# Kernel tuning notes

Hardware: AMD Instinct MI355X
Metric: run time of the kernel (lower is better)

## Reference

```python
import jax, jax.numpy as jnp
import numpy as np

NUM_EXPERTS = 8


def setup_inputs() -> dict:
    key = jax.random.key(0)
    k1, k2, k3, k4, k5 = jax.random.split(key, 5)
    T, D, DFF, E, K = 2048, 2048, 1024, NUM_EXPERTS, 2
    hidden_states = jax.random.normal(k1, (T, D), dtype=jnp.float32)
    w1 = jax.random.normal(k2, (E, 2 * DFF, D), dtype=jnp.float32) * 0.02
    w2 = jax.random.normal(k3, (E, D, DFF), dtype=jnp.float32) * 0.02
    topk_weights = jax.random.uniform(k4, (T, K), dtype=jnp.float32)
    topk_weights = topk_weights / jnp.sum(topk_weights, axis=-1, keepdims=True)
    topk_ids = jax.random.randint(k5, (T, K), 0, E, dtype=jnp.int32)
    return {"hidden_states": hidden_states, "w1": w1, "w2": w2,
            "topk_weights": topk_weights, "topk_ids": topk_ids}


def _expert_fn(x, w1_e, w2_e):
    # x: [T, D], w1_e: [2*DFF, D], w2_e: [D, DFF]
    gu = x @ w1_e.T                      # [T, 2*DFF]
    dff = w2_e.shape[1]
    gate, up = gu[:, :dff], gu[:, dff:]
    h = jax.nn.silu(gate) * up           # SiLU-and-mul activation
    return h @ w2_e.T                    # [T, D]


def reference(hidden_states, w1, w2, topk_weights, topk_ids):
    T = hidden_states.shape[0]
    E = w1.shape[0]
    # route[t, e] = sum_k topk_weights[t,k] * (topk_ids[t,k] == e)
    route = jnp.zeros((T, E), dtype=hidden_states.dtype)
    route = route.at[jnp.arange(T)[:, None], topk_ids].add(topk_weights)
    # per-expert dense GEMMs (E is small and fixed), then weighted combine
    outs = jax.vmap(lambda w1_e, w2_e: _expert_fn(hidden_states, w1_e, w2_e))(w1, w2)  # [E, T, D]
    return jnp.einsum('te,etd->td', route, outs)
```

## Files before the change

kernel.cpp:

```cpp
#include <hip/hip_runtime.h>
#include <hip/hip_bf16.h>
#include <stdint.h>

typedef __attribute__((ext_vector_type(4))) float f32x4;
typedef __attribute__((ext_vector_type(8))) short bf16x8;
typedef unsigned short u16;

#define T_TOK   2048
#define D_DIM   2048
#define DFF_DIM 1024
#define NEXP    8
#define TOPK    2
#define NROWS   (T_TOK * TOPK)
#define BM      128
#define BK      64
#define MAX_MB  40
#define GRID_G  (16 * MAX_MB)
#define CVT2_BLKS 256

#define XB_OFF    65536
#define XB_BYTES  ((size_t)T_TOK * D_DIM * 2)
#define H_OFF     (XB_OFF + XB_BYTES)
#define H_BYTES   ((size_t)NROWS * DFF_DIM * 2)
#define W1B_OFF   (H_OFF + H_BYTES)
#define W1B_BYTES ((size_t)NEXP * 2 * DFF_DIM * D_DIM * 2)
#define W2B_OFF   (W1B_OFF + W1B_BYTES)
#define W2B_BYTES ((size_t)NEXP * D_DIM * DFF_DIM * 2)
#define WS_NEED   (W2B_OFF + W2B_BYTES)

#define W1_T   ((size_t)NEXP * 2 * DFF_DIM * D_DIM / 8)
#define W2_T   ((size_t)NEXP * D_DIM * DFF_DIM / 8)
#define X_T    ((size_t)T_TOK * D_DIM / 8)
#define PREP_CHUNKS_A (W1_T + X_T)
#define PREP_BLKS 2048

#define PIN() asm volatile("" ::: "memory")
#define BAR_LGKM()                                                        \
    asm volatile("s_waitcnt lgkmcnt(0)" ::: "memory");                    \
    __builtin_amdgcn_s_barrier()

__device__ __forceinline__ u16 f2bf(float f) {
    __hip_bfloat16 h = __float2bfloat16(f);
    return *reinterpret_cast<u16*>(&h);
}

__device__ __forceinline__ void cvt8(const float* src, u16* dst) {
    f32x4 a = *(const f32x4*)src;
    f32x4 b = *(const f32x4*)(src + 4);
    bf16x8 v;
#pragma unroll
    for (int j = 0; j < 4; ++j) { v[j] = (short)f2bf(a[j]); v[j + 4] = (short)f2bf(b[j]); }
    *(bf16x8*)dst = v;
}

__device__ __forceinline__ void cvt8_nt(const float* src, u16* dst) {
    f32x4 a = __builtin_nontemporal_load((const f32x4*)src);
    f32x4 b = __builtin_nontemporal_load(((const f32x4*)src) + 1);
    bf16x8 v;
#pragma unroll
    for (int j = 0; j < 4; ++j) { v[j] = (short)f2bf(a[j]); v[j + 4] = (short)f2bf(b[j]); }
    *(bf16x8*)dst = v;
}

__device__ __forceinline__ void gll16(const u16* gsrc, const u16* lds) {
    __builtin_amdgcn_global_load_lds(
        (const __attribute__((address_space(1))) uint32_t*)gsrc,
        (__attribute__((address_space(3))) uint32_t*)lds, 16, 0, 0);
}

__device__ __forceinline__ bf16x8 lds_read8_swz(const u16* base, int row, int inner) {
    int off = row * 128 + (inner ^ ((row & 7) << 4));
    return *(const bf16x8*)((const char*)base + off);
}

__device__ __forceinline__ void route_body(const int* topk_ids, const float* topk_w,
                                           int* sched, int* row_token, float* row_w,
                                           int* cnt, int* off, int* cur) {
    const int tid = threadIdx.x;
    if (tid < NEXP) cnt[tid] = 0;
    __syncthreads();
    for (int p = tid; p < NROWS; p += blockDim.x)
        atomicAdd(&cnt[topk_ids[p]], 1);
    __syncthreads();
    if (tid == 0) {
        int acc = 0, mb = 0;
        for (int e = 0; e < NEXP; ++e) {
            off[e] = acc;
            int c = cnt[e];
            for (int m0 = 0; m0 < c; m0 += BM) {
                sched[1 + 3 * mb] = e;
                sched[2 + 3 * mb] = acc + m0;
                sched[3 + 3 * mb] = (c - m0 < BM) ? (c - m0) : BM;
                ++mb;
            }
            acc += c;
        }
        sched[0] = mb;
    }
    if (tid < NEXP) cur[tid] = 0;
    __syncthreads();
    for (int p = tid; p < NROWS; p += blockDim.x) {
        int e = topk_ids[p];
        int slot = off[e] + atomicAdd(&cur[e], 1);
        row_token[slot] = p / TOPK;
        row_w[slot]     = topk_w[p];
    }
}

__global__ void prep_kernel(const float* __restrict__ w1, const float* __restrict__ X,
                            u16* __restrict__ w1b, u16* __restrict__ Xb,
                            float* __restrict__ out,
                            const int* __restrict__ topk_ids,
                            const float* __restrict__ topk_w,
                            int* __restrict__ sched, int* __restrict__ row_token,
                            float* __restrict__ row_w) {
    __shared__ int cnt[NEXP], off[NEXP], cur[NEXP];
    if (blockIdx.x == PREP_BLKS) {
        route_body(topk_ids, topk_w, sched, row_token, row_w, cnt, off, cur);
        return;
    }
    const size_t stride = (size_t)PREP_BLKS * 256;
    for (size_t t = (size_t)blockIdx.x * 256 + threadIdx.x; t < PREP_CHUNKS_A; t += stride) {
        if (t < W1_T) {
            cvt8_nt(w1 + t * 8, w1b + t * 8);
        } else {
            size_t u = t - W1_T;
            cvt8_nt(X + u * 8, Xb + u * 8);
            f32x4 z = (f32x4){0.f, 0.f, 0.f, 0.f};
            *(f32x4*)(out + u * 8) = z;
            *(f32x4*)(out + u * 8 + 4) = z;
        }
    }
}

#define DECODE_BLOCK()                                                    \
    const int bid   = blockIdx.x;                                         \
    const int xcd   = bid & 7;                                            \
    const int local = bid >> 3;                                \
    const int n0h   = local / MAX_MB;                          \
    const int mb    = local - n0h * MAX_MB;                               \
    const int n0i   = xcd * 2 + n0h;                           \
    if (mb >= sched[0]) return;                                           \
    const int e    = sched[1 + 3 * mb];                                   \
    const int m0   = sched[2 + 3 * mb];                                   \
    const int mlen = sched[3 + 3 * mb]

#define GLL8(k0)                                                          \
    _Pragma("unroll") for (int i = 0; i < 4; ++i)                         \
        gll16(asrc[i] + (k0), &lA[aoff[i]]);                              \
    _Pragma("unroll") for (int i = 0; i < 4; ++i)                         \
        gll16(bsrc[i] + (k0), &lB[aoff[i]]);

__global__ __launch_bounds__(256, 3)
void gemm1p_kernel(const u16* __restrict__ Xb, const u16* __restrict__ w1b,
                   const int* __restrict__ sched, const int* __restrict__ row_token,
                   u16* __restrict__ H,
                   const float* __restrict__ w2f, u16* __restrict__ w2b) {
    __shared__ u16 lA[BM * BK];
    __shared__ u16 lB[BM * BK];

    if (blockIdx.x >= GRID_G) {
        const size_t stride = (size_t)CVT2_BLKS * 256;
        for (size_t t = (size_t)(blockIdx.x - GRID_G) * 256 + threadIdx.x;
             t < W2_T; t += stride)
            cvt8_nt(w2f + t * 8, w2b + t * 8);
        return;
    }

    DECODE_BLOCK();
    const int n0 = n0i * 64;

    const int tid  = threadIdx.x;
    const int lane = tid & 63;
    const int wave = tid >> 6;
    const int wm = wave >> 1, wn = wave & 1;
    const int lr = lane & 15, lk = lane >> 4;

    const u16* asrc[4];
    const u16* bsrc[4];
    int aoff[4];
#pragma unroll
    for (int i = 0; i < 4; ++i) {
        int R = i * 32 + wave * 8 + (lane >> 3);
        int grow = m0 + R; if (grow > NROWS - 1) grow = NROWS - 1;
        int tok = row_token[grow];
        int c8 = ((lane & 7) ^ (R & 7)) * 8;
        asrc[i] = Xb + (size_t)tok * D_DIM + c8;
        int gr = (R < 64) ? (n0 + R) : (DFF_DIM + n0 + (R - 64));
        bsrc[i] = w1b + ((size_t)e * (2 * DFF_DIM) + gr) * D_DIM + c8;
        aoff[i] = i * 2048 + wave * 512;
    }

    f32x4 accg[4][2], accu[4][2];
#pragma unroll
    for (int m = 0; m < 4; ++m)
#pragma unroll
        for (int n = 0; n < 2; ++n) {
            accg[m][n] = (f32x4){0.f, 0.f, 0.f, 0.f};
            accu[m][n] = (f32x4){0.f, 0.f, 0.f, 0.f};
        }

    const int KT = D_DIM / BK;
    for (int kt = 0; kt < KT; ++kt) {
        GLL8(kt * BK);
        __syncthreads();
#pragma unroll
        for (int ks = 0; ks < 2; ++ks) {
            const int inner = ks * 64 + lk * 16;
            bf16x8 af[4], bg[2], bu[2];
#pragma unroll
            for (int m = 0; m < 4; ++m)
                af[m] = lds_read8_swz(lA, wm * 64 + m * 16 + lr, inner);
#pragma unroll
            for (int n = 0; n < 2; ++n) {
                bg[n] = lds_read8_swz(lB, wn * 32 + n * 16 + lr, inner);
                bu[n] = lds_read8_swz(lB, 64 + wn * 32 + n * 16 + lr, inner);
            }
#pragma unroll
            for (int m = 0; m < 4; ++m)
#pragma unroll
                for (int n = 0; n < 2; ++n) {
                    accg[m][n] = __builtin_amdgcn_mfma_f32_16x16x32_bf16(af[m], bg[n], accg[m][n], 0, 0, 0);
                    accu[m][n] = __builtin_amdgcn_mfma_f32_16x16x32_bf16(af[m], bu[n], accu[m][n], 0, 0, 0);
                }
        }
        __syncthreads();
    }

#pragma unroll
    for (int m = 0; m < 4; ++m)
#pragma unroll
        for (int n = 0; n < 2; ++n)
#pragma unroll
            for (int r = 0; r < 4; ++r) {
                int rloc = wm * 64 + m * 16 + (lane >> 4) * 4 + r;
                if (rloc < mlen) {
                    int col = wn * 32 + n * 16 + lr;
                    float g = accg[m][n][r], u = accu[m][n][r];
                    float h = (g / (1.f + __expf(-g))) * u;
                    H[(size_t)(m0 + rloc) * DFF_DIM + n0 + col] = f2bf(h);
                }
            }
}

__global__ __launch_bounds__(256, 3)
void gemm2p_kernel(const u16* __restrict__ H, const u16* __restrict__ w2b,
                   const int* __restrict__ sched, const int* __restrict__ row_token,
                   const float* __restrict__ row_w, float* __restrict__ out) {
    __shared__ u16 lA[BM * BK];
    __shared__ u16 lB[BM * BK];

    DECODE_BLOCK();
    const int n0 = n0i * 128;

    const int tid  = threadIdx.x;
    const int lane = tid & 63;
    const int wave = tid >> 6;
    const int wm = wave >> 1, wn = wave & 1;
    const int lr = lane & 15, lk = lane >> 4;

    const u16* asrc[4];
    const u16* bsrc[4];
    int aoff[4];
#pragma unroll
    for (int i = 0; i < 4; ++i) {
        int R = i * 32 + wave * 8 + (lane >> 3);
        int grow = m0 + R; if (grow > NROWS - 1) grow = NROWS - 1;
        int c8 = ((lane & 7) ^ (R & 7)) * 8;
        asrc[i] = H + (size_t)grow * DFF_DIM + c8;
        bsrc[i] = w2b + ((size_t)e * D_DIM + (n0 + R)) * DFF_DIM + c8;
        aoff[i] = i * 2048 + wave * 512;
    }

    f32x4 acc[4][4];
#pragma unroll
    for (int m = 0; m < 4; ++m)
#pragma unroll
        for (int n = 0; n < 4; ++n) acc[m][n] = (f32x4){0.f, 0.f, 0.f, 0.f};

    const int KT = DFF_DIM / BK;
    for (int kt = 0; kt < KT; ++kt) {
        GLL8(kt * BK);
        __syncthreads();
#pragma unroll
        for (int ks = 0; ks < 2; ++ks) {
            const int inner = ks * 64 + lk * 16;
            bf16x8 af[4], bfr[4];
#pragma unroll
            for (int m = 0; m < 4; ++m)
                af[m] = lds_read8_swz(lA, wm * 64 + m * 16 + lr, inner);
#pragma unroll
            for (int n = 0; n < 4; ++n)
                bfr[n] = lds_read8_swz(lB, wn * 64 + n * 16 + lr, inner);
#pragma unroll
            for (int m = 0; m < 4; ++m)
#pragma unroll
                for (int n = 0; n < 4; ++n)
                    acc[m][n] = __builtin_amdgcn_mfma_f32_16x16x32_bf16(af[m], bfr[n], acc[m][n], 0, 0, 0);
        }
        __syncthreads();
    }

#pragma unroll
    for (int m = 0; m < 4; ++m)
#pragma unroll
        for (int n = 0; n < 4; ++n)
#pragma unroll
            for (int r = 0; r < 4; ++r) {
                int rloc = wm * 64 + m * 16 + (lane >> 4) * 4 + r;
                if (rloc < mlen) {
                    int grow = m0 + rloc;
                    int tok  = row_token[grow];
                    float w  = row_w[grow];
                    int col  = wn * 64 + n * 16 + lr;
                    atomicAdd(&out[(size_t)tok * D_DIM + n0 + col], acc[m][n][r] * w);
                }
            }
}

__global__ void cvt_x_kernel(const float* __restrict__ X, u16* __restrict__ Xb,
                             float* __restrict__ out) {
    int idx = (blockIdx.x * 256 + threadIdx.x) * 8;
    cvt8(X + idx, Xb + idx);
    f32x4 z = (f32x4){0.f, 0.f, 0.f, 0.f};
    *(f32x4*)(out + idx) = z;
    *(f32x4*)(out + idx + 4) = z;
}

__global__ void route_kernel(const int* __restrict__ topk_ids,
                             const float* __restrict__ topk_w,
                             int* __restrict__ sched,
                             int* __restrict__ row_token,
                             float* __restrict__ row_w) {
    __shared__ int cnt[NEXP], off[NEXP], cur[NEXP];
    route_body(topk_ids, topk_w, sched, row_token, row_w, cnt, off, cur);
}

#define GLL_A(k0, dst)                                                    \
    _Pragma("unroll") for (int i = 0; i < 4; ++i)                         \
        gll16(asrc[i] + (k0), &(dst)[aoff[i]]);

#define LOAD_RB(rb, k0)                                                   \
    _Pragma("unroll") for (int i = 0; i < 4; ++i) {                       \
        rb[i][0] = *(const f32x4*)(bptr[i] + (k0));                       \
        rb[i][1] = *(const f32x4*)(bptr[i] + (k0) + 4);                   \
    }

#define CVT_WRITE(rb, dst)                                                \
    _Pragma("unroll") for (int i = 0; i < 4; ++i) {                       \
        bf16x8 vb;                                                        \
        _Pragma("unroll") for (int j = 0; j < 4; ++j) {                   \
            vb[j] = (short)f2bf(rb[i][0][j]);                             \
            vb[j + 4] = (short)f2bf(rb[i][1][j]);                         \
        }                                                                 \
        *(bf16x8*)((char*)(dst) + wroff[i]) = vb;                         \
    }

__global__ __launch_bounds__(256, 3)
void gemm1f_kernel(const u16* __restrict__ Xb, const float* __restrict__ w1,
                   const int* __restrict__ sched, const int* __restrict__ row_token,
                   u16* __restrict__ H) {
    __shared__ u16 lA[2][BM * BK];
    __shared__ u16 lB[BM * BK];

    DECODE_BLOCK();
    const int n0 = n0i * 64;

    const int tid  = threadIdx.x;
    const int lane = tid & 63;
    const int wave = tid >> 6;
    const int wm = wave >> 1, wn = wave & 1;
    const int lr = lane & 15, lk = lane >> 4;

    const u16* asrc[4];
    int aoff[4];
#pragma unroll
    for (int i = 0; i < 4; ++i) {
        int R = i * 32 + wave * 8 + (lane >> 3);
        int grow = m0 + R; if (grow > NROWS - 1) grow = NROWS - 1;
        int tok = row_token[grow];
        asrc[i] = Xb + (size_t)tok * D_DIM + (size_t)(((lane & 7) ^ (R & 7)) * 8);
        aoff[i] = i * 2048 + wave * 512;
    }
    const float* bptr[4];
    int wroff[4];
#pragma unroll
    for (int i = 0; i < 4; ++i) {
        int chunk = i * 256 + tid;
        int row = chunk >> 3, c8 = chunk & 7;
        int gcol = (row < 64) ? (n0 + row) : (DFF_DIM + n0 + (row - 64));
        bptr[i] = w1 + ((size_t)e * (2 * DFF_DIM) + gcol) * D_DIM + c8 * 8;
        wroff[i] = row * 128 + ((c8 * 16) ^ ((row & 7) << 4));
    }

    f32x4 rb[4][2];
    f32x4 accg[4][2], accu[4][2];
#pragma unroll
    for (int m = 0; m < 4; ++m)
#pragma unroll
        for (int n = 0; n < 2; ++n) {
            accg[m][n] = (f32x4){0.f, 0.f, 0.f, 0.f};
            accu[m][n] = (f32x4){0.f, 0.f, 0.f, 0.f};
        }

#define MFMA_G1(bufA, bufB)                                               \
    _Pragma("unroll") for (int ks = 0; ks < 2; ++ks) {                    \
        const int inner = ks * 64 + lk * 16;                              \
        bf16x8 af[4], bg[2], bu[2];                                       \
        _Pragma("unroll") for (int m = 0; m < 4; ++m)                     \
            af[m] = lds_read8_swz(bufA, wm * 64 + m * 16 + lr, inner);    \
        _Pragma("unroll") for (int n = 0; n < 2; ++n) {                   \
            bg[n] = lds_read8_swz(bufB, wn * 32 + n * 16 + lr, inner);    \
            bu[n] = lds_read8_swz(bufB, 64 + wn * 32 + n * 16 + lr, inner); \
        }                                                                 \
        _Pragma("unroll") for (int m = 0; m < 4; ++m)                     \
            _Pragma("unroll") for (int n = 0; n < 2; ++n) {               \
                accg[m][n] = __builtin_amdgcn_mfma_f32_16x16x32_bf16(af[m], bg[n], accg[m][n], 0, 0, 0); \
                accu[m][n] = __builtin_amdgcn_mfma_f32_16x16x32_bf16(af[m], bu[n], accu[m][n], 0, 0, 0); \
            }                                                             \
    }

    const int KT = D_DIM / BK;
    LOAD_RB(rb, 0);
    GLL_A(0, lA[0]);
    CVT_WRITE(rb, lB);
    __syncthreads();

    for (int kt = 0, cur = 0; kt < KT; ++kt, cur ^= 1) {
        if (kt + 1 < KT) {
            LOAD_RB(rb, (kt + 1) * BK);
            GLL_A((kt + 1) * BK, lA[cur ^ 1]);
        }
        PIN();
        MFMA_G1(lA[cur], lB);
        BAR_LGKM();
        if (kt + 1 < KT) { CVT_WRITE(rb, lB); }
        __syncthreads();
    }
#undef MFMA_G1

#pragma unroll
    for (int m = 0; m < 4; ++m)
#pragma unroll
        for (int n = 0; n < 2; ++n)
#pragma unroll
            for (int r = 0; r < 4; ++r) {
                int rloc = wm * 64 + m * 16 + (lane >> 4) * 4 + r;
                if (rloc < mlen) {
                    int col = wn * 32 + n * 16 + lr;
                    float g = accg[m][n][r], u = accu[m][n][r];
                    float h = (g / (1.f + __expf(-g))) * u;
                    H[(size_t)(m0 + rloc) * DFF_DIM + n0 + col] = f2bf(h);
                }
            }
}

__global__ __launch_bounds__(256, 3)
void gemm2f_kernel(const u16* __restrict__ H, const float* __restrict__ w2,
                   const int* __restrict__ sched, const int* __restrict__ row_token,
                   const float* __restrict__ row_w, float* __restrict__ out) {
    __shared__ u16 lA[2][BM * BK];
    __shared__ u16 lB[BM * BK];

    DECODE_BLOCK();
    const int n0 = n0i * 128;

    const int tid  = threadIdx.x;
    const int lane = tid & 63;
    const int wave = tid >> 6;
    const int wm = wave >> 1, wn = wave & 1;
    const int lr = lane & 15, lk = lane >> 4;

    const u16* asrc[4];
    int aoff[4];
#pragma unroll
    for (int i = 0; i < 4; ++i) {
        int R = i * 32 + wave * 8 + (lane >> 3);
        int grow = m0 + R; if (grow > NROWS - 1) grow = NROWS - 1;
        asrc[i] = H + (size_t)grow * DFF_DIM + (size_t)(((lane & 7) ^ (R & 7)) * 8);
        aoff[i] = i * 2048 + wave * 512;
    }
    const float* bptr[4];
    int wroff[4];
#pragma unroll
    for (int i = 0; i < 4; ++i) {
        int chunk = i * 256 + tid;
        int row = chunk >> 3, c8 = chunk & 7;
        bptr[i] = w2 + ((size_t)e * D_DIM + (n0 + row)) * DFF_DIM + c8 * 8;
        wroff[i] = row * 128 + ((c8 * 16) ^ ((row & 7) << 4));
    }

    f32x4 rb[4][2];
    f32x4 acc[4][4];
#pragma unroll
    for (int m = 0; m < 4; ++m)
#pragma unroll
        for (int n = 0; n < 4; ++n) acc[m][n] = (f32x4){0.f, 0.f, 0.f, 0.f};

#define MFMA_G2(bufA, bufB)                                               \
    _Pragma("unroll") for (int ks = 0; ks < 2; ++ks) {                    \
        const int inner = ks * 64 + lk * 16;                              \
        bf16x8 af[4], bfr[4];                                             \
        _Pragma("unroll") for (int m = 0; m < 4; ++m)                     \
            af[m] = lds_read8_swz(bufA, wm * 64 + m * 16 + lr, inner);    \
        _Pragma("unroll") for (int n = 0; n < 4; ++n)                     \
            bfr[n] = lds_read8_swz(bufB, wn * 64 + n * 16 + lr, inner);   \
        _Pragma("unroll") for (int m = 0; m < 4; ++m)                     \
            _Pragma("unroll") for (int n = 0; n < 4; ++n)                 \
                acc[m][n] = __builtin_amdgcn_mfma_f32_16x16x32_bf16(af[m], bfr[n], acc[m][n], 0, 0, 0); \
    }

    const int KT = DFF_DIM / BK;
    LOAD_RB(rb, 0);
    GLL_A(0, lA[0]);
    CVT_WRITE(rb, lB);
    __syncthreads();

    for (int kt = 0, cur = 0; kt < KT; ++kt, cur ^= 1) {
        if (kt + 1 < KT) {
            LOAD_RB(rb, (kt + 1) * BK);
            GLL_A((kt + 1) * BK, lA[cur ^ 1]);
        }
        PIN();
        MFMA_G2(lA[cur], lB);
        BAR_LGKM();
        if (kt + 1 < KT) { CVT_WRITE(rb, lB); }
        __syncthreads();
    }
#undef MFMA_G2

#pragma unroll
    for (int m = 0; m < 4; ++m)
#pragma unroll
        for (int n = 0; n < 4; ++n)
#pragma unroll
            for (int r = 0; r < 4; ++r) {
                int rloc = wm * 64 + m * 16 + (lane >> 4) * 4 + r;
                if (rloc < mlen) {
                    int grow = m0 + rloc;
                    int tok  = row_token[grow];
                    float w  = row_w[grow];
                    int col  = wn * 64 + n * 16 + lr;
                    atomicAdd(&out[(size_t)tok * D_DIM + n0 + col], acc[m][n][r] * w);
                }
            }
}

extern "C" void kernel_launch(void* const* d_in, const int* in_sizes, int n_in,
                              void* d_out, int out_size, void* d_ws, size_t ws_size,
                              hipStream_t stream) {
    const float* X  = (const float*)d_in[0];
    const float* w1 = (const float*)d_in[1];
    const float* w2 = (const float*)d_in[2];
    const float* tw = (const float*)d_in[3];
    const int*   ti = (const int*)d_in[4];

    int*   sched     = (int*)d_ws;
    int*   row_token = (int*)((char*)d_ws + 512);
    float* row_w     = (float*)((char*)d_ws + 512 + 4 * NROWS);
    u16*   Xb        = (u16*)((char*)d_ws + XB_OFF);
    u16*   H         = (u16*)((char*)d_ws + H_OFF);

    if (ws_size >= WS_NEED) {
        u16* w1b = (u16*)((char*)d_ws + W1B_OFF);
        u16* w2b = (u16*)((char*)d_ws + W2B_OFF);
        prep_kernel<<<PREP_BLKS + 1, 256, 0, stream>>>(w1, X, w1b, Xb,
                                                       (float*)d_out, ti, tw,
                                                       sched, row_token, row_w);
        gemm1p_kernel<<<GRID_G + CVT2_BLKS, 256, 0, stream>>>(Xb, w1b, sched, row_token, H,
                                                              w2, w2b);
        gemm2p_kernel<<<GRID_G, 256, 0, stream>>>(H, w2b, sched, row_token, row_w, (float*)d_out);
    } else {
        route_kernel<<<1, 256, 0, stream>>>(ti, tw, sched, row_token, row_w);
        cvt_x_kernel<<<(T_TOK * D_DIM) / (256 * 8), 256, 0, stream>>>(X, Xb, (float*)d_out);
        gemm1f_kernel<<<GRID_G, 256, 0, stream>>>(Xb, w1, sched, row_token, H);
        gemm2f_kernel<<<GRID_G, 256, 0, stream>>>(H, w2, sched, row_token, row_w, (float*)d_out);
    }
}
```

Baseline: 164.1 us.

## Drop W1 pre-conversion pass; convert fp32 W1 inside gemm1 while overlapping W2 convert

Removes the separate pass that converted all of W1 from fp32 to bf16 in the prep kernel. The first GEMM now reads fp32 W1 directly, using the former fallback kernel, which is extended to convert W2 in extra blocks. This avoids writing and re-reading a full bf16 copy of W1, cutting global memory traffic, in exchange for in-GEMM conversion cost and reading W1 at fp32 width. The W2 conversion block count drops from 256 to 64 and the prep kernel now only converts X.

```diff
diff --git a/kernel.cpp b/kernel.cpp
--- a/kernel.cpp
+++ b/kernel.cpp
@@ -16,23 +16,19 @@
 #define BK      64
 #define MAX_MB  40
 #define GRID_G  (16 * MAX_MB)
-#define CVT2_BLKS 256
+#define CVT2_BLKS 64
 
 #define XB_OFF    65536
 #define XB_BYTES  ((size_t)T_TOK * D_DIM * 2)
 #define H_OFF     (XB_OFF + XB_BYTES)
 #define H_BYTES   ((size_t)NROWS * DFF_DIM * 2)
-#define W1B_OFF   (H_OFF + H_BYTES)
-#define W1B_BYTES ((size_t)NEXP * 2 * DFF_DIM * D_DIM * 2)
-#define W2B_OFF   (W1B_OFF + W1B_BYTES)
+#define W2B_OFF   (H_OFF + H_BYTES)
 #define W2B_BYTES ((size_t)NEXP * D_DIM * DFF_DIM * 2)
 #define WS_NEED   (W2B_OFF + W2B_BYTES)
 
-#define W1_T   ((size_t)NEXP * 2 * DFF_DIM * D_DIM / 8)
 #define W2_T   ((size_t)NEXP * D_DIM * DFF_DIM / 8)
 #define X_T    ((size_t)T_TOK * D_DIM / 8)
-#define PREP_CHUNKS_A (W1_T + X_T)
-#define PREP_BLKS 2048
+#define PREPX_BLKS 512
 
 #define PIN() asm volatile("" ::: "memory")
 #define BAR_LGKM()                                                        \
@@ -107,29 +103,23 @@
     }
 }
 
-__global__ void prep_kernel(const float* __restrict__ w1, const float* __restrict__ X,
-                            u16* __restrict__ w1b, u16* __restrict__ Xb,
-                            float* __restrict__ out,
+__global__ void prep_kernel(const float* __restrict__ X,
+                            u16* __restrict__ Xb, float* __restrict__ out,
                             const int* __restrict__ topk_ids,
                             const float* __restrict__ topk_w,
                             int* __restrict__ sched, int* __restrict__ row_token,
                             float* __restrict__ row_w) {
     __shared__ int cnt[NEXP], off[NEXP], cur[NEXP];
-    if (blockIdx.x == PREP_BLKS) {
+    if (blockIdx.x == PREPX_BLKS) {
         route_body(topk_ids, topk_w, sched, row_token, row_w, cnt, off, cur);
         return;
     }
-    const size_t stride = (size_t)PREP_BLKS * 256;
-    for (size_t t = (size_t)blockIdx.x * 256 + threadIdx.x; t < PREP_CHUNKS_A; t += stride) {
-        if (t < W1_T) {
-            cvt8_nt(w1 + t * 8, w1b + t * 8);
-        } else {
-            size_t u = t - W1_T;
-            cvt8_nt(X + u * 8, Xb + u * 8);
-            f32x4 z = (f32x4){0.f, 0.f, 0.f, 0.f};
-            *(f32x4*)(out + u * 8) = z;
-            *(f32x4*)(out + u * 8 + 4) = z;
-        }
+    const size_t stride = (size_t)PREPX_BLKS * 256;
+    for (size_t t = (size_t)blockIdx.x * 256 + threadIdx.x; t < X_T; t += stride) {
+        cvt8_nt(X + t * 8, Xb + t * 8);
+        f32x4 z = (f32x4){0.f, 0.f, 0.f, 0.f};
+        *(f32x4*)(out + t * 8) = z;
+        *(f32x4*)(out + t * 8 + 4) = z;
     }
 }
 
@@ -145,197 +135,6 @@
     const int m0   = sched[2 + 3 * mb];                                   \
     const int mlen = sched[3 + 3 * mb]
 
-#define GLL8(k0)                                                          \
-    _Pragma("unroll") for (int i = 0; i < 4; ++i)                         \
-        gll16(asrc[i] + (k0), &lA[aoff[i]]);                              \
-    _Pragma("unroll") for (int i = 0; i < 4; ++i)                         \
-        gll16(bsrc[i] + (k0), &lB[aoff[i]]);
-
-__global__ __launch_bounds__(256, 3)
-void gemm1p_kernel(const u16* __restrict__ Xb, const u16* __restrict__ w1b,
-                   const int* __restrict__ sched, const int* __restrict__ row_token,
-                   u16* __restrict__ H,
-                   const float* __restrict__ w2f, u16* __restrict__ w2b) {
-    __shared__ u16 lA[BM * BK];
-    __shared__ u16 lB[BM * BK];
-
-    if (blockIdx.x >= GRID_G) {
-        const size_t stride = (size_t)CVT2_BLKS * 256;
-        for (size_t t = (size_t)(blockIdx.x - GRID_G) * 256 + threadIdx.x;
-             t < W2_T; t += stride)
-            cvt8_nt(w2f + t * 8, w2b + t * 8);
-        return;
-    }
-
-    DECODE_BLOCK();
-    const int n0 = n0i * 64;
-
-    const int tid  = threadIdx.x;
-    const int lane = tid & 63;
-    const int wave = tid >> 6;
-    const int wm = wave >> 1, wn = wave & 1;
-    const int lr = lane & 15, lk = lane >> 4;
-
-    const u16* asrc[4];
-    const u16* bsrc[4];
-    int aoff[4];
-#pragma unroll
-    for (int i = 0; i < 4; ++i) {
-        int R = i * 32 + wave * 8 + (lane >> 3);
-        int grow = m0 + R; if (grow > NROWS - 1) grow = NROWS - 1;
-        int tok = row_token[grow];
-        int c8 = ((lane & 7) ^ (R & 7)) * 8;
-        asrc[i] = Xb + (size_t)tok * D_DIM + c8;
-        int gr = (R < 64) ? (n0 + R) : (DFF_DIM + n0 + (R - 64));
-        bsrc[i] = w1b + ((size_t)e * (2 * DFF_DIM) + gr) * D_DIM + c8;
-        aoff[i] = i * 2048 + wave * 512;
-    }
-
-    f32x4 accg[4][2], accu[4][2];
-#pragma unroll
-    for (int m = 0; m < 4; ++m)
-#pragma unroll
-        for (int n = 0; n < 2; ++n) {
-            accg[m][n] = (f32x4){0.f, 0.f, 0.f, 0.f};
-            accu[m][n] = (f32x4){0.f, 0.f, 0.f, 0.f};
-        }
-
-    const int KT = D_DIM / BK;
-    for (int kt = 0; kt < KT; ++kt) {
-        GLL8(kt * BK);
-        __syncthreads();
-#pragma unroll
-        for (int ks = 0; ks < 2; ++ks) {
-            const int inner = ks * 64 + lk * 16;
-            bf16x8 af[4], bg[2], bu[2];
-#pragma unroll
-            for (int m = 0; m < 4; ++m)
-                af[m] = lds_read8_swz(lA, wm * 64 + m * 16 + lr, inner);
-#pragma unroll
-            for (int n = 0; n < 2; ++n) {
-                bg[n] = lds_read8_swz(lB, wn * 32 + n * 16 + lr, inner);
-                bu[n] = lds_read8_swz(lB, 64 + wn * 32 + n * 16 + lr, inner);
-            }
-#pragma unroll
-            for (int m = 0; m < 4; ++m)
-#pragma unroll
-                for (int n = 0; n < 2; ++n) {
-                    accg[m][n] = __builtin_amdgcn_mfma_f32_16x16x32_bf16(af[m], bg[n], accg[m][n], 0, 0, 0);
-                    accu[m][n] = __builtin_amdgcn_mfma_f32_16x16x32_bf16(af[m], bu[n], accu[m][n], 0, 0, 0);
-                }
-        }
-        __syncthreads();
-    }
-
-#pragma unroll
-    for (int m = 0; m < 4; ++m)
-#pragma unroll
-        for (int n = 0; n < 2; ++n)
-#pragma unroll
-            for (int r = 0; r < 4; ++r) {
-                int rloc = wm * 64 + m * 16 + (lane >> 4) * 4 + r;
-                if (rloc < mlen) {
-                    int col = wn * 32 + n * 16 + lr;
-                    float g = accg[m][n][r], u = accu[m][n][r];
-                    float h = (g / (1.f + __expf(-g))) * u;
-                    H[(size_t)(m0 + rloc) * DFF_DIM + n0 + col] = f2bf(h);
-                }
-            }
-}
-
-__global__ __launch_bounds__(256, 3)
-void gemm2p_kernel(const u16* __restrict__ H, const u16* __restrict__ w2b,
-                   const int* __restrict__ sched, const int* __restrict__ row_token,
-                   const float* __restrict__ row_w, float* __restrict__ out) {
-    __shared__ u16 lA[BM * BK];
-    __shared__ u16 lB[BM * BK];
-
-    DECODE_BLOCK();
-    const int n0 = n0i * 128;
-
-    const int tid  = threadIdx.x;
-    const int lane = tid & 63;
-    const int wave = tid >> 6;
-    const int wm = wave >> 1, wn = wave & 1;
-    const int lr = lane & 15, lk = lane >> 4;
-
-    const u16* asrc[4];
-    const u16* bsrc[4];
-    int aoff[4];
-#pragma unroll
-    for (int i = 0; i < 4; ++i) {
-        int R = i * 32 + wave * 8 + (lane >> 3);
-        int grow = m0 + R; if (grow > NROWS - 1) grow = NROWS - 1;
-        int c8 = ((lane & 7) ^ (R & 7)) * 8;
-        asrc[i] = H + (size_t)grow * DFF_DIM + c8;
-        bsrc[i] = w2b + ((size_t)e * D_DIM + (n0 + R)) * DFF_DIM + c8;
-        aoff[i] = i * 2048 + wave * 512;
-    }
-
-    f32x4 acc[4][4];
-#pragma unroll
-    for (int m = 0; m < 4; ++m)
-#pragma unroll
-        for (int n = 0; n < 4; ++n) acc[m][n] = (f32x4){0.f, 0.f, 0.f, 0.f};
-
-    const int KT = DFF_DIM / BK;
-    for (int kt = 0; kt < KT; ++kt) {
-        GLL8(kt * BK);
-        __syncthreads();
-#pragma unroll
-        for (int ks = 0; ks < 2; ++ks) {
-            const int inner = ks * 64 + lk * 16;
-            bf16x8 af[4], bfr[4];
-#pragma unroll
-            for (int m = 0; m < 4; ++m)
-                af[m] = lds_read8_swz(lA, wm * 64 + m * 16 + lr, inner);
-#pragma unroll
-            for (int n = 0; n < 4; ++n)
-                bfr[n] = lds_read8_swz(lB, wn * 64 + n * 16 + lr, inner);
-#pragma unroll
-            for (int m = 0; m < 4; ++m)
-#pragma unroll
-                for (int n = 0; n < 4; ++n)
-                    acc[m][n] = __builtin_amdgcn_mfma_f32_16x16x32_bf16(af[m], bfr[n], acc[m][n], 0, 0, 0);
-        }
-        __syncthreads();
-    }
-
-#pragma unroll
-    for (int m = 0; m < 4; ++m)
-#pragma unroll
-        for (int n = 0; n < 4; ++n)
-#pragma unroll
-            for (int r = 0; r < 4; ++r) {
-                int rloc = wm * 64 + m * 16 + (lane >> 4) * 4 + r;
-                if (rloc < mlen) {
-                    int grow = m0 + rloc;
-                    int tok  = row_token[grow];
-                    float w  = row_w[grow];
-                    int col  = wn * 64 + n * 16 + lr;
-                    atomicAdd(&out[(size_t)tok * D_DIM + n0 + col], acc[m][n][r] * w);
-                }
-            }
-}
-
-__global__ void cvt_x_kernel(const float* __restrict__ X, u16* __restrict__ Xb,
-                             float* __restrict__ out) {
-    int idx = (blockIdx.x * 256 + threadIdx.x) * 8;
-    cvt8(X + idx, Xb + idx);
-    f32x4 z = (f32x4){0.f, 0.f, 0.f, 0.f};
-    *(f32x4*)(out + idx) = z;
-    *(f32x4*)(out + idx + 4) = z;
-}
-
-__global__ void route_kernel(const int* __restrict__ topk_ids,
-                             const float* __restrict__ topk_w,
-                             int* __restrict__ sched,
-                             int* __restrict__ row_token,
-                             float* __restrict__ row_w) {
-    __shared__ int cnt[NEXP], off[NEXP], cur[NEXP];
-    route_body(topk_ids, topk_w, sched, row_token, row_w, cnt, off, cur);
-}
-
 #define GLL_A(k0, dst)                                                    \
     _Pragma("unroll") for (int i = 0; i < 4; ++i)                         \
         gll16(asrc[i] + (k0), &(dst)[aoff[i]]);
@@ -357,11 +156,20 @@
     }
 
 __global__ __launch_bounds__(256, 3)
-void gemm1f_kernel(const u16* __restrict__ Xb, const float* __restrict__ w1,
+void gemm1h_kernel(const u16* __restrict__ Xb, const float* __restrict__ w1,
                    const int* __restrict__ sched, const int* __restrict__ row_token,
-                   u16* __restrict__ H) {
+                   u16* __restrict__ H,
+                   const float* __restrict__ w2f, u16* __restrict__ w2b) {
     __shared__ u16 lA[2][BM * BK];
     __shared__ u16 lB[BM * BK];
+
+    if (blockIdx.x >= GRID_G) {
+        const size_t stride = (size_t)CVT2_BLKS * 256;
+        for (size_t t = (size_t)(blockIdx.x - GRID_G) * 256 + threadIdx.x;
+             t < W2_T; t += stride)
+            cvt8_nt(w2f + t * 8, w2b + t * 8);
+        return;
+    }
 
     DECODE_BLOCK();
     const int n0 = n0i * 64;
@@ -456,6 +264,84 @@
 }
 
 __global__ __launch_bounds__(256, 3)
+void gemm2p_kernel(const u16* __restrict__ H, const u16* __restrict__ w2b,
+                   const int* __restrict__ sched, const int* __restrict__ row_token,
+                   const float* __restrict__ row_w, float* __restrict__ out) {
+    __shared__ u16 lA[BM * BK];
+    __shared__ u16 lB[BM * BK];
+
+    DECODE_BLOCK();
+    const int n0 = n0i * 128;
+
+    const int tid  = threadIdx.x;
+    const int lane = tid & 63;
+    const int wave = tid >> 6;
+    const int wm = wave >> 1, wn = wave & 1;
+    const int lr = lane & 15, lk = lane >> 4;
+
+    const u16* asrc[4];
+    const u16* bsrc[4];
+    int aoff[4];
+#pragma unroll
+    for (int i = 0; i < 4; ++i) {
+        int R = i * 32 + wave * 8 + (lane >> 3);
+        int grow = m0 + R; if (grow > NROWS - 1) grow = NROWS - 1;
+        int c8 = ((lane & 7) ^ (R & 7)) * 8;
+        asrc[i] = H + (size_t)grow * DFF_DIM + c8;
+        bsrc[i] = w2b + ((size_t)e * D_DIM + (n0 + R)) * DFF_DIM + c8;
+        aoff[i] = i * 2048 + wave * 512;
+    }
+
+    f32x4 acc[4][4];
+#pragma unroll
+    for (int m = 0; m < 4; ++m)
+#pragma unroll
+        for (int n = 0; n < 4; ++n) acc[m][n] = (f32x4){0.f, 0.f, 0.f, 0.f};
+
+    const int KT = DFF_DIM / BK;
+    for (int kt = 0; kt < KT; ++kt) {
+#pragma unroll
+        for (int i = 0; i < 4; ++i) gll16(asrc[i] + kt * BK, &lA[aoff[i]]);
+#pragma unroll
+        for (int i = 0; i < 4; ++i) gll16(bsrc[i] + kt * BK, &lB[aoff[i]]);
+        __syncthreads();
+#pragma unroll
+        for (int ks = 0; ks < 2; ++ks) {
+            const int inner = ks * 64 + lk * 16;
+            bf16x8 af[4], bfr[4];
+#pragma unroll
+            for (int m = 0; m < 4; ++m)
+                af[m] = lds_read8_swz(lA, wm * 64 + m * 16 + lr, inner);
+#pragma unroll
+            for (int n = 0; n < 4; ++n)
+                bfr[n] = lds_read8_swz(lB, wn * 64 + n * 16 + lr, inner);
+#pragma unroll
+            for (int m = 0; m < 4; ++m)
+#pragma unroll
+                for (int n = 0; n < 4; ++n)
+                    acc[m][n] = __builtin_amdgcn_mfma_f32_16x16x32_bf16(af[m], bfr[n], acc[m][n], 0, 0, 0);
+        }
+        __syncthreads();
+    }
+
+#pragma unroll
+    for (int m = 0; m < 4; ++m)
+#pragma unroll
+        for (int n = 0; n < 4; ++n)
+#pragma unroll
+            for (int r = 0; r < 4; ++r) {
+                int rloc = wm * 64 + m * 16 + (lane >> 4) * 4 + r;
+                if (rloc < mlen) {
+                    int grow = m0 + rloc;
+                    int tok  = row_token[grow];
+                    float w  = row_w[grow];
+                    int col  = wn * 64 + n * 16 + lr;
+                    atomicAdd(&out[(size_t)tok * D_DIM + n0 + col], acc[m][n][r] * w);
+                }
+            }
+}
+
+__global__ __launch_bounds__(256, 3)
 void gemm2f_kernel(const u16* __restrict__ H, const float* __restrict__ w2,
                    const int* __restrict__ sched, const int* __restrict__ row_token,
                    const float* __restrict__ row_w, float* __restrict__ out) {
@@ -561,19 +447,16 @@
     u16*   Xb        = (u16*)((char*)d_ws + XB_OFF);
     u16*   H         = (u16*)((char*)d_ws + H_OFF);
 
+    prep_kernel<<<PREPX_BLKS + 1, 256, 0, stream>>>(X, Xb, (float*)d_out,
+                                                    ti, tw, sched, row_token, row_w);
     if (ws_size >= WS_NEED) {
-        u16* w1b = (u16*)((char*)d_ws + W1B_OFF);
         u16* w2b = (u16*)((char*)d_ws + W2B_OFF);
-        prep_kernel<<<PREP_BLKS + 1, 256, 0, stream>>>(w1, X, w1b, Xb,
-                                                       (float*)d_out, ti, tw,
-                                                       sched, row_token, row_w);
-        gemm1p_kernel<<<GRID_G + CVT2_BLKS, 256, 0, stream>>>(Xb, w1b, sched, row_token, H,
-                                                              w2, w2b);
+        gemm1h_kernel<<<GRID_G + CVT2_BLKS, 256, 0, stream>>>(Xb, w1, sched, row_token,
+                                                              H, w2, w2b);
         gemm2p_kernel<<<GRID_G, 256, 0, stream>>>(H, w2b, sched, row_token, row_w, (float*)d_out);
     } else {
-        route_kernel<<<1, 256, 0, stream>>>(ti, tw, sched, row_token, row_w);
-        cvt_x_kernel<<<(T_TOK * D_DIM) / (256 * 8), 256, 0, stream>>>(X, Xb, (float*)d_out);
-        gemm1f_kernel<<<GRID_G, 256, 0, stream>>>(Xb, w1, sched, row_token, H);
+        gemm1h_kernel<<<GRID_G, 256, 0, stream>>>(Xb, w1, sched, row_token,
+                                                  H, w2, (u16*)nullptr);
         gemm2f_kernel<<<GRID_G, 256, 0, stream>>>(H, w2, sched, row_token, row_w, (float*)d_out);
     }
 }
```

After: 178.5 us. 8.7% more time.
